# Performance work log

Hardware: AMD Instinct MI355X
Metric: run time of the kernel (lower is better)

The kernel has to match this reference:

```python
import jax, jax.numpy as jnp
import numpy as np

R = 32
LORA_ALPHA = 64
SCALING = LORA_ALPHA / R  # 2.0
TOPK = 2
NOISE_EPS = 0.01


def setup_inputs() -> dict:
    key = jax.random.key(0)
    ks = jax.random.split(key, 7)
    B, S, D, OUT, E = 4, 2048, 4096, 4096, 8
    x = jax.random.normal(ks[0], (B, S, D), dtype=jnp.float32)
    eof_index = jax.random.randint(ks[1], (B,), 0, S)
    noise = jax.random.normal(ks[2], (B, E), dtype=jnp.float32)
    # learned params (random instead of the zero-init in reset_parameters so the
    # output is non-trivial); Linear weight layout is [out_features, in_features]
    A_w = jax.random.normal(ks[3], (R, D), dtype=jnp.float32) * (1.0 / np.sqrt(D))
    B_w = jax.random.normal(ks[4], (E, OUT, R), dtype=jnp.float32) * (1.0 / np.sqrt(R))
    route_w = jax.random.normal(ks[5], (E, D), dtype=jnp.float32) * (1.0 / np.sqrt(D))
    noise_w = jax.random.normal(ks[6], (E, D), dtype=jnp.float32) * (1.0 / np.sqrt(D))
    return {"x": x, "eof_index": eof_index, "noise": noise,
            "A_w": A_w, "B_w": B_w, "route_w": route_w, "noise_w": noise_w}


def reference(x, eof_index, noise, A_w, B_w, route_w, noise_w):
    B = x.shape[0]
    rows = jnp.arange(B)
    # routing input: token at eof_index for each batch row -> [B, D]
    routing_input = x[rows, eof_index]
    # noisy top-k gating (training path: noisy_gating and is_train are True)
    clean_logits = routing_input @ route_w.T                       # [B, E]
    noise_stddev = jax.nn.softplus(routing_input @ noise_w.T) + NOISE_EPS
    logits = clean_logits + noise * noise_stddev                   # [B, E]
    # torch code takes topk+1 then slices to topk; equivalent to top_k(topk)
    top_vals, top_idx = jax.lax.top_k(logits, TOPK)                # [B, K]
    top_gates = jax.nn.softmax(top_vals.astype(jnp.float32), axis=-1).astype(x.dtype)
    gates = jnp.zeros_like(logits).at[rows[:, None], top_idx].set(top_gates)  # [B, E]
    # shared low-rank projection
    shared = jnp.einsum('bsd,rd->bsr', x, A_w)                     # [B, S, r]
    # sum_i gate_i * (shared @ B_i^T), fused as one contraction
    lora_output = jnp.einsum('bsr,eor,be->bso', shared, B_w, gates)  # [B, S, out]
    return lora_output * SCALING
```

## Files before the change

### kernel.cpp

```cpp
#include <hip/hip_runtime.h>
#include <stdint.h>
#include <math.h>

#define B_ 4
#define S_ 2048
#define D_ 4096
#define O_ 4096
#define E_ 8
#define R_ 32
#define SCALING 2.0f
#define NOISE_EPS 0.01f

typedef unsigned short u16;
typedef short s16x8 __attribute__((ext_vector_type(8)));
typedef float f32x4 __attribute__((ext_vector_type(4)));

__device__ __forceinline__ float b2f(u16 u) {
  union { unsigned int i; float f; } v; v.i = ((unsigned int)u) << 16; return v.f;
}
__device__ __forceinline__ u16 f2b(float f) {
  union { unsigned int i; float f; } v; v.f = f;
  unsigned int i = v.i;
  return (u16)((i + 0x7FFFu + ((i >> 16) & 1u)) >> 16);
}
__device__ __forceinline__ void split2(float f, u16* h, u16* l) {
  u16 hi = f2b(f);
  *h = hi;
  *l = f2b(f - b2f(hi));
}

__device__ __forceinline__ float ld(const void* p, size_t i, int bf) {
  return bf ? b2f(((const u16*)p)[i]) : ((const float*)p)[i];
}

__global__ void k_detect(const unsigned int* __restrict__ xw, int* __restrict__ flag) {
  __shared__ int cnt;
  if (threadIdx.x == 0) cnt = 0;
  __syncthreads();
  unsigned int w = xw[threadIdx.x];
  unsigned int e = (w >> 7) & 0xFFu;
  if (e >= 90u && e <= 140u) atomicAdd(&cnt, 1);
  __syncthreads();
  if (threadIdx.x == 0) *flag = (cnt > 48) ? 1 : 0;
}

__global__ __launch_bounds__(256) void k_logits(
    const void* __restrict__ x, const int* __restrict__ eof,
    const void* __restrict__ route_w, const void* __restrict__ noise_w,
    const int* __restrict__ flag, float* __restrict__ wsf) {
  int bf = *flag;
  int be = blockIdx.x;
  int b = be >> 3, e = be & 7;
  size_t xoff = ((size_t)b * S_ + (size_t)eof[b]) * D_;
  size_t woff = (size_t)e * D_;
  float ac = 0.f, an = 0.f;
  for (int d = threadIdx.x; d < D_; d += 256) {
    float xv = ld(x, xoff + d, bf);
    ac += xv * ld(route_w, woff + d, bf);
    an += xv * ld(noise_w, woff + d, bf);
  }
  __shared__ float rc[256], rn[256];
  rc[threadIdx.x] = ac; rn[threadIdx.x] = an;
  __syncthreads();
  for (int s = 128; s > 0; s >>= 1) {
    if (threadIdx.x < (unsigned)s) {
      rc[threadIdx.x] += rc[threadIdx.x + s];
      rn[threadIdx.x] += rn[threadIdx.x + s];
    }
    __syncthreads();
  }
  if (threadIdx.x == 0) { wsf[16 + be] = rc[0]; wsf[48 + be] = rn[0]; }
}

__global__ void k_gates(const void* __restrict__ noise, const int* __restrict__ flag,
                        float* __restrict__ wsf) {
  int bf = *flag;
  int b = threadIdx.x;
  if (b >= B_) return;
  float lg[E_];
  for (int e = 0; e < E_; e++) {
    float c = wsf[16 + b * 8 + e];
    float n = wsf[48 + b * 8 + e];
    float sp = (n > 20.f) ? n : log1pf(expf(n));
    lg[e] = c + ld(noise, b * 8 + e, bf) * (sp + NOISE_EPS);
  }
  int i1 = 0; float v1 = lg[0];
  for (int e = 1; e < E_; e++) if (lg[e] > v1) { v1 = lg[e]; i1 = e; }
  int i2 = -1; float v2 = -3.0e38f;
  for (int e = 0; e < E_; e++) if (e != i1 && lg[e] > v2) { v2 = lg[e]; i2 = e; }
  float t = expf(v2 - v1);
  float g1 = 1.f / (1.f + t);
  float g2 = t / (1.f + t);
  for (int e = 0; e < E_; e++) wsf[80 + b * 8 + e] = 0.f;
  wsf[80 + b * 8 + i1] = g1;
  wsf[80 + b * 8 + i2] = g2;
}

__global__ __launch_bounds__(256) void k_prepA(
    const float* __restrict__ Aw, const int* __restrict__ flag,
    u16* __restrict__ A2h, u16* __restrict__ A2l) {
  if (*flag) return;
  int idx = blockIdx.x * 256 + threadIdx.x;
  f32x4 v = ((const f32x4*)Aw)[idx];
  ushort4 h, l;
  split2(v[0], &h.x, &l.x); split2(v[1], &h.y, &l.y);
  split2(v[2], &h.z, &l.z); split2(v[3], &h.w, &l.w);
  ((ushort4*)A2h)[idx] = h;
  ((ushort4*)A2l)[idx] = l;
}

__global__ __launch_bounds__(256) void k_wc(
    const void* __restrict__ Bw, const int* __restrict__ flag,
    const float* __restrict__ gates, u16* __restrict__ Wc2h,
    u16* __restrict__ Wc2l) {
  int bf = *flag;
  int idx = blockIdx.x * 256 + threadIdx.x;
  int b = idx >> 15;
  int u = idx & 32767;
  float g[E_];
#pragma unroll
  for (int e = 0; e < E_; e++) g[e] = gates[b * 8 + e];
  f32x4 acc = {0.f, 0.f, 0.f, 0.f};
  if (bf) {
#pragma unroll
    for (int e = 0; e < E_; e++) {
      ushort4 v = ((const ushort4*)Bw)[(size_t)e * 32768 + u];
      acc[0] += g[e] * b2f(v.x);
      acc[1] += g[e] * b2f(v.y);
      acc[2] += g[e] * b2f(v.z);
      acc[3] += g[e] * b2f(v.w);
    }
  } else {
#pragma unroll
    for (int e = 0; e < E_; e++) {
      f32x4 v = ((const f32x4*)Bw)[(size_t)e * 32768 + u];
      acc += g[e] * v;
    }
  }
  acc *= SCALING;
  ushort4 h, l;
  split2(acc[0], &h.x, &l.x); split2(acc[1], &h.y, &l.y);
  split2(acc[2], &h.z, &l.z); split2(acc[3], &h.w, &l.w);
  ((ushort4*)Wc2h)[idx] = h;
  ((ushort4*)Wc2l)[idx] = l;
}

__global__ __launch_bounds__(256) void k_sharedM(
    const void* __restrict__ xv, const void* __restrict__ Awv,
    const u16* __restrict__ A2h, const u16* __restrict__ A2l,
    const int* __restrict__ flag, u16* __restrict__ sh2h,
    u16* __restrict__ sh2l) {
  __shared__ float red[4][512];
  int bf = *flag;
  int lane = threadIdx.x & 63;
  int wave = threadIdx.x >> 6;
  int m = lane & 15, kg = lane >> 4;
  int row0 = blockIdx.x * 16;
  int kbase = wave * 1024 + kg * 8;
  f32x4 acc0 = {0.f, 0.f, 0.f, 0.f};
  f32x4 acc1 = {0.f, 0.f, 0.f, 0.f};
  if (bf) {
    const u16* xp = (const u16*)xv + (size_t)(row0 + m) * D_ + kbase;
    const u16* a0 = (const u16*)Awv + (size_t)m * D_ + kbase;
    const u16* a1 = (const u16*)Awv + (size_t)(m + 16) * D_ + kbase;
#pragma unroll 4
    for (int k0 = 0; k0 < 1024; k0 += 32) {
      s16x8 a  = *(const s16x8*)(xp + k0);
      s16x8 b0 = *(const s16x8*)(a0 + k0);
      s16x8 b1 = *(const s16x8*)(a1 + k0);
      acc0 = __builtin_amdgcn_mfma_f32_16x16x32_bf16(a, b0, acc0, 0, 0, 0);
      acc1 = __builtin_amdgcn_mfma_f32_16x16x32_bf16(a, b1, acc1, 0, 0, 0);
    }
  } else {
    const float* xp = (const float*)xv + (size_t)(row0 + m) * D_ + kbase;
    const u16* h0 = A2h + (size_t)m * D_ + kbase;
    const u16* l0 = A2l + (size_t)m * D_ + kbase;
    const u16* h1 = A2h + (size_t)(m + 16) * D_ + kbase;
    const u16* l1 = A2l + (size_t)(m + 16) * D_ + kbase;
#pragma unroll 2
    for (int k0 = 0; k0 < 1024; k0 += 32) {
      f32x4 x0 = *(const f32x4*)(xp + k0);
      f32x4 x1 = *(const f32x4*)(xp + k0 + 4);
      s16x8 xh, xl;
      u16 hh, ll;
#pragma unroll
      for (int j = 0; j < 4; j++) {
        split2(x0[j], &hh, &ll); xh[j] = (short)hh; xl[j] = (short)ll;
        split2(x1[j], &hh, &ll); xh[j + 4] = (short)hh; xl[j + 4] = (short)ll;
      }
      s16x8 bh0 = *(const s16x8*)(h0 + k0);
      s16x8 bl0 = *(const s16x8*)(l0 + k0);
      s16x8 bh1 = *(const s16x8*)(h1 + k0);
      s16x8 bl1 = *(const s16x8*)(l1 + k0);
      acc0 = __builtin_amdgcn_mfma_f32_16x16x32_bf16(xh, bh0, acc0, 0, 0, 0);
      acc0 = __builtin_amdgcn_mfma_f32_16x16x32_bf16(xh, bl0, acc0, 0, 0, 0);
      acc0 = __builtin_amdgcn_mfma_f32_16x16x32_bf16(xl, bh0, acc0, 0, 0, 0);
      acc1 = __builtin_amdgcn_mfma_f32_16x16x32_bf16(xh, bh1, acc1, 0, 0, 0);
      acc1 = __builtin_amdgcn_mfma_f32_16x16x32_bf16(xh, bl1, acc1, 0, 0, 0);
      acc1 = __builtin_amdgcn_mfma_f32_16x16x32_bf16(xl, bh1, acc1, 0, 0, 0);
    }
  }
  int crow = (lane >> 4) * 4, ccol = lane & 15;
#pragma unroll
  for (int j = 0; j < 4; j++) {
    red[wave][(crow + j) * 32 + ccol]      = acc0[j];
    red[wave][(crow + j) * 32 + ccol + 16] = acc1[j];
  }
  __syncthreads();
  int t = threadIdx.x;
#pragma unroll
  for (int q = 0; q < 2; q++) {
    int e = t + q * 256;
    float s = red[0][e] + red[1][e] + red[2][e] + red[3][e];
    u16 h, l;
    split2(s, &h, &l);
    sh2h[(size_t)row0 * R_ + e] = h;
    sh2l[(size_t)row0 * R_ + e] = l;
  }
}

__global__ __launch_bounds__(256) void k_outM(
    const u16* __restrict__ sh2h, const u16* __restrict__ sh2l,
    const u16* __restrict__ Wc2h, const u16* __restrict__ Wc2l,
    const int* __restrict__ flag, void* __restrict__ out) {
  int bf = *flag;
  int lane = threadIdx.x & 63;
  int wave = threadIdx.x >> 6;
  int rb = blockIdx.x >> 5;
  int ob = blockIdx.x & 31;
  int row0 = rb * 64 + wave * 16;
  int b = row0 >> 11;
  int m = lane & 15, kg = lane >> 4;
  s16x8 Ah = *(const s16x8*)(sh2h + (size_t)(row0 + m) * R_ + kg * 8);
  s16x8 Al = *(const s16x8*)(sh2l + (size_t)(row0 + m) * R_ + kg * 8);
  const u16* wh = Wc2h + (size_t)b * (O_ * R_) + (size_t)(ob * 128 + m) * R_ + kg * 8;
  const u16* wl = Wc2l + (size_t)b * (O_ * R_) + (size_t)(ob * 128 + m) * R_ + kg * 8;
  int crow = (lane >> 4) * 4;
#pragma unroll
  for (int ot = 0; ot < 8; ot++) {
    s16x8 Bh = *(const s16x8*)(wh + (size_t)ot * 16 * R_);
    s16x8 Bl = *(const s16x8*)(wl + (size_t)ot * 16 * R_);
    f32x4 acc = {0.f, 0.f, 0.f, 0.f};
    acc = __builtin_amdgcn_mfma_f32_16x16x32_bf16(Ah, Bh, acc, 0, 0, 0);
    acc = __builtin_amdgcn_mfma_f32_16x16x32_bf16(Ah, Bl, acc, 0, 0, 0);
    acc = __builtin_amdgcn_mfma_f32_16x16x32_bf16(Al, Bh, acc, 0, 0, 0);
    int o = ob * 128 + ot * 16 + m;
    if (bf) {
      u16* op = (u16*)out + (size_t)(row0 + crow) * O_ + o;
#pragma unroll
      for (int j = 0; j < 4; j++) op[(size_t)j * O_] = f2b(acc[j]);
    } else {
      float* op = (float*)out + (size_t)(row0 + crow) * O_ + o;
#pragma unroll
      for (int j = 0; j < 4; j++) op[(size_t)j * O_] = acc[j];
    }
  }
}

extern "C" void kernel_launch(void* const* d_in, const int* in_sizes, int n_in,
                              void* d_out, int out_size, void* d_ws, size_t ws_size,
                              hipStream_t stream) {
  const void* x       = d_in[0];
  const int*  eof     = (const int*)d_in[1];
  const void* noise   = d_in[2];
  const void* Aw      = d_in[3];
  const void* Bw      = d_in[4];
  const void* route_w = d_in[5];
  const void* noise_w = d_in[6];
  float* wsf = (float*)d_ws;
  int* flag = (int*)wsf;
  float* gates = wsf + 80;
  u16* Wc2h = (u16*)(wsf + 112);
  u16* Wc2l = Wc2h + (size_t)B_ * O_ * R_;
  u16* A2h  = Wc2l + (size_t)B_ * O_ * R_;
  u16* A2l  = A2h + (size_t)R_ * D_;
  u16* sh2h = A2l + (size_t)R_ * D_;
  u16* sh2l = sh2h + (size_t)B_ * S_ * R_;

  k_detect<<<1, 64, 0, stream>>>((const unsigned int*)x, flag);
  k_logits<<<B_ * E_, 256, 0, stream>>>(x, eof, route_w, noise_w, flag, wsf);
  k_gates<<<1, 64, 0, stream>>>(noise, flag, wsf);
  k_prepA<<<(R_ * D_ / 4) / 256, 256, 0, stream>>>((const float*)Aw, flag, A2h, A2l);
  k_wc<<<(B_ * O_ * R_ / 4) / 256, 256, 0, stream>>>(Bw, flag, gates, Wc2h, Wc2l);
  k_sharedM<<<(B_ * S_) / 16, 256, 0, stream>>>(x, Aw, A2h, A2l, flag, sh2h, sh2l);
  k_outM<<<((B_ * S_) / 64) * (O_ / 128), 256, 0, stream>>>(
      sh2h, sh2l, Wc2h, Wc2l, flag, d_out);
}
```

Measured before the change: 318.5 us.

## Prepack MFMA operand layouts, stage x through swizzled LDS, coalesce output stores

A and the gate-combined B weights are now written in MFMA fragment order, so each lane reads its 16-byte operand contiguously. k_sharedM stages fp32 x rows into swizzled LDS as bf16 hi/lo with coalesced global reads. It then runs the split-bf16 MFMA chain over k-chunks, and writes shared in fragment layout. k_outM now handles 16 rows per block across all output columns, staging results in LDS so stores are wide and coalesced. The cost is extra block barriers and LDS use, plus a different grid shape.

```diff
diff --git a/kernel.cpp b/kernel.cpp
--- a/kernel.cpp
+++ b/kernel.cpp
@@ -98,25 +98,38 @@
 
 __global__ __launch_bounds__(256) void k_prepA(
     const float* __restrict__ Aw, const int* __restrict__ flag,
-    u16* __restrict__ A2h, u16* __restrict__ A2l) {
+    u16* __restrict__ Aph, u16* __restrict__ Apl) {
   if (*flag) return;
-  int idx = blockIdx.x * 256 + threadIdx.x;
-  f32x4 v = ((const f32x4*)Aw)[idx];
-  ushort4 h, l;
-  split2(v[0], &h.x, &l.x); split2(v[1], &h.y, &l.y);
-  split2(v[2], &h.z, &l.z); split2(v[3], &h.w, &l.w);
-  ((ushort4*)A2h)[idx] = h;
-  ((ushort4*)A2l)[idx] = l;
+  int flat = blockIdx.x * 256 + threadIdx.x;
+  int k32idx = flat >> 7;
+  int rem = flat & 127;
+  int h = rem >> 6;
+  int lane = rem & 63;
+  int r = h * 16 + (lane & 15);
+  int d = k32idx * 32 + (lane >> 4) * 8;
+  const float* src = Aw + (size_t)r * D_ + d;
+  f32x4 v0 = *(const f32x4*)src;
+  f32x4 v1 = *(const f32x4*)(src + 4);
+  ushort4 h0, l0, h1, l1;
+  split2(v0[0], &h0.x, &l0.x); split2(v0[1], &h0.y, &l0.y);
+  split2(v0[2], &h0.z, &l0.z); split2(v0[3], &h0.w, &l0.w);
+  split2(v1[0], &h1.x, &l1.x); split2(v1[1], &h1.y, &l1.y);
+  split2(v1[2], &h1.z, &l1.z); split2(v1[3], &h1.w, &l1.w);
+  *(ushort4*)(Aph + (size_t)flat * 8)     = h0;
+  *(ushort4*)(Aph + (size_t)flat * 8 + 4) = h1;
+  *(ushort4*)(Apl + (size_t)flat * 8)     = l0;
+  *(ushort4*)(Apl + (size_t)flat * 8 + 4) = l1;
 }
 
 __global__ __launch_bounds__(256) void k_wc(
     const void* __restrict__ Bw, const int* __restrict__ flag,
-    const float* __restrict__ gates, u16* __restrict__ Wc2h,
-    u16* __restrict__ Wc2l) {
+    const float* __restrict__ gates, u16* __restrict__ Wph,
+    u16* __restrict__ Wpl) {
   int bf = *flag;
   int idx = blockIdx.x * 256 + threadIdx.x;
   int b = idx >> 15;
   int u = idx & 32767;
+  int o = u >> 3, rq = u & 7;
   float g[E_];
 #pragma unroll
   for (int e = 0; e < E_; e++) g[e] = gates[b * 8 + e];
@@ -141,25 +154,31 @@
   ushort4 h, l;
   split2(acc[0], &h.x, &l.x); split2(acc[1], &h.y, &l.y);
   split2(acc[2], &h.z, &l.z); split2(acc[3], &h.w, &l.w);
-  ((ushort4*)Wc2h)[idx] = h;
-  ((ushort4*)Wc2l)[idx] = l;
+  int ot = o >> 4;
+  int lane = ((rq >> 1) * 16) + (o & 15);
+  size_t base = (((size_t)b * 256 + ot) * 64 + lane) * 8 + (rq & 1) * 4;
+  *(ushort4*)(Wph + base) = h;
+  *(ushort4*)(Wpl + base) = l;
 }
 
 __global__ __launch_bounds__(256) void k_sharedM(
     const void* __restrict__ xv, const void* __restrict__ Awv,
-    const u16* __restrict__ A2h, const u16* __restrict__ A2l,
+    const u16* __restrict__ Aph, const u16* __restrict__ Apl,
     const int* __restrict__ flag, u16* __restrict__ sh2h,
     u16* __restrict__ sh2l) {
+  __shared__ u16 xh[4096];
+  __shared__ u16 xl[4096];
   __shared__ float red[4][512];
   int bf = *flag;
-  int lane = threadIdx.x & 63;
-  int wave = threadIdx.x >> 6;
+  int t = threadIdx.x;
+  int lane = t & 63;
+  int wave = t >> 6;
   int m = lane & 15, kg = lane >> 4;
   int row0 = blockIdx.x * 16;
-  int kbase = wave * 1024 + kg * 8;
   f32x4 acc0 = {0.f, 0.f, 0.f, 0.f};
   f32x4 acc1 = {0.f, 0.f, 0.f, 0.f};
   if (bf) {
+    int kbase = wave * 1024 + kg * 8;
     const u16* xp = (const u16*)xv + (size_t)(row0 + m) * D_ + kbase;
     const u16* a0 = (const u16*)Awv + (size_t)m * D_ + kbase;
     const u16* a1 = (const u16*)Awv + (size_t)(m + 16) * D_ + kbase;
@@ -172,33 +191,45 @@
       acc1 = __builtin_amdgcn_mfma_f32_16x16x32_bf16(a, b1, acc1, 0, 0, 0);
     }
   } else {
-    const float* xp = (const float*)xv + (size_t)(row0 + m) * D_ + kbase;
-    const u16* h0 = A2h + (size_t)m * D_ + kbase;
-    const u16* l0 = A2l + (size_t)m * D_ + kbase;
-    const u16* h1 = A2h + (size_t)(m + 16) * D_ + kbase;
-    const u16* l1 = A2l + (size_t)(m + 16) * D_ + kbase;
-#pragma unroll 2
-    for (int k0 = 0; k0 < 1024; k0 += 32) {
-      f32x4 x0 = *(const f32x4*)(xp + k0);
-      f32x4 x1 = *(const f32x4*)(xp + k0 + 4);
-      s16x8 xh, xl;
-      u16 hh, ll;
-#pragma unroll
-      for (int j = 0; j < 4; j++) {
-        split2(x0[j], &hh, &ll); xh[j] = (short)hh; xl[j] = (short)ll;
-        split2(x1[j], &hh, &ll); xh[j + 4] = (short)hh; xl[j + 4] = (short)ll;
+    int srow = t >> 4;
+    int sq = t & 15;
+    const float* xrow = (const float*)xv + (size_t)(row0 + srow) * D_;
+    for (int kc = 0; kc < D_; kc += 256) {
+      __syncthreads();
+#pragma unroll
+      for (int q = 0; q < 4; q++) {
+        int colf = (sq + q * 16) * 4;
+        f32x4 v = *(const f32x4*)(xrow + kc + colf);
+        ushort4 h, l;
+        split2(v[0], &h.x, &l.x); split2(v[1], &h.y, &l.y);
+        split2(v[2], &h.z, &l.z); split2(v[3], &h.w, &l.w);
+        int swz = (srow * 512 + colf * 2) ^ ((srow & 7) << 4);
+        *(ushort4*)((char*)xh + swz) = h;
+        *(ushort4*)((char*)xl + swz) = l;
       }
-      s16x8 bh0 = *(const s16x8*)(h0 + k0);
-      s16x8 bl0 = *(const s16x8*)(l0 + k0);
-      s16x8 bh1 = *(const s16x8*)(h1 + k0);
-      s16x8 bl1 = *(const s16x8*)(l1 + k0);
-      acc0 = __builtin_amdgcn_mfma_f32_16x16x32_bf16(xh, bh0, acc0, 0, 0, 0);
-      acc0 = __builtin_amdgcn_mfma_f32_16x16x32_bf16(xh, bl0, acc0, 0, 0, 0);
-      acc0 = __builtin_amdgcn_mfma_f32_16x16x32_bf16(xl, bh0, acc0, 0, 0, 0);
-      acc1 = __builtin_amdgcn_mfma_f32_16x16x32_bf16(xh, bh1, acc1, 0, 0, 0);
-      acc1 = __builtin_amdgcn_mfma_f32_16x16x32_bf16(xh, bl1, acc1, 0, 0, 0);
-      acc1 = __builtin_amdgcn_mfma_f32_16x16x32_bf16(xl, bh1, acc1, 0, 0, 0);
-    }
+      __syncthreads();
+#pragma unroll
+      for (int p = 0; p < 2; p++) {
+        int k32 = (wave * 2 + p) * 32;
+        int boff = (m * 512 + (k32 + kg * 8) * 2) ^ ((m & 7) << 4);
+        s16x8 ah = *(const s16x8*)((const char*)xh + boff);
+        s16x8 al = *(const s16x8*)((const char*)xl + boff);
+        size_t k32idx = (size_t)(kc >> 5) + wave * 2 + p;
+        const u16* ph = Aph + (k32idx * 2) * 512;
+        const u16* pl = Apl + (k32idx * 2) * 512;
+        s16x8 bh0 = *(const s16x8*)(ph + (size_t)lane * 8);
+        s16x8 bl0 = *(const s16x8*)(pl + (size_t)lane * 8);
+        s16x8 bh1 = *(const s16x8*)(ph + 512 + (size_t)lane * 8);
+        s16x8 bl1 = *(const s16x8*)(pl + 512 + (size_t)lane * 8);
+        acc0 = __builtin_amdgcn_mfma_f32_16x16x32_bf16(ah, bh0, acc0, 0, 0, 0);
+        acc0 = __builtin_amdgcn_mfma_f32_16x16x32_bf16(ah, bl0, acc0, 0, 0, 0);
+        acc0 = __builtin_amdgcn_mfma_f32_16x16x32_bf16(al, bh0, acc0, 0, 0, 0);
+        acc1 = __builtin_amdgcn_mfma_f32_16x16x32_bf16(ah, bh1, acc1, 0, 0, 0);
+        acc1 = __builtin_amdgcn_mfma_f32_16x16x32_bf16(ah, bl1, acc1, 0, 0, 0);
+        acc1 = __builtin_amdgcn_mfma_f32_16x16x32_bf16(al, bh1, acc1, 0, 0, 0);
+      }
+    }
+    __syncthreads();
   }
   int crow = (lane >> 4) * 4, ccol = lane & 15;
 #pragma unroll
@@ -207,53 +238,67 @@
     red[wave][(crow + j) * 32 + ccol + 16] = acc1[j];
   }
   __syncthreads();
-  int t = threadIdx.x;
 #pragma unroll
   for (int q = 0; q < 2; q++) {
     int e = t + q * 256;
     float s = red[0][e] + red[1][e] + red[2][e] + red[3][e];
     u16 h, l;
     split2(s, &h, &l);
-    sh2h[(size_t)row0 * R_ + e] = h;
-    sh2l[(size_t)row0 * R_ + e] = l;
-  }
-}
-
+    int row = e >> 5, r = e & 31;
+    size_t dst = (size_t)blockIdx.x * 512 + ((size_t)(r >> 3) * 16 + row) * 8 + (r & 7);
+    sh2h[dst] = h;
+    sh2l[dst] = l;
+  }
+}
+
+#define OCH 512
 __global__ __launch_bounds__(256) void k_outM(
     const u16* __restrict__ sh2h, const u16* __restrict__ sh2l,
-    const u16* __restrict__ Wc2h, const u16* __restrict__ Wc2l,
+    const u16* __restrict__ Wph, const u16* __restrict__ Wpl,
     const int* __restrict__ flag, void* __restrict__ out) {
-  int bf = *flag;
-  int lane = threadIdx.x & 63;
-  int wave = threadIdx.x >> 6;
-  int rb = blockIdx.x >> 5;
-  int ob = blockIdx.x & 31;
-  int row0 = rb * 64 + wave * 16;
+  __shared__ float C[16][516];
+  int bf = *flag;
+  int t = threadIdx.x;
+  int lane = t & 63, wave = t >> 6;
+  int row0 = blockIdx.x * 16;
   int b = row0 >> 11;
-  int m = lane & 15, kg = lane >> 4;
-  s16x8 Ah = *(const s16x8*)(sh2h + (size_t)(row0 + m) * R_ + kg * 8);
-  s16x8 Al = *(const s16x8*)(sh2l + (size_t)(row0 + m) * R_ + kg * 8);
-  const u16* wh = Wc2h + (size_t)b * (O_ * R_) + (size_t)(ob * 128 + m) * R_ + kg * 8;
-  const u16* wl = Wc2l + (size_t)b * (O_ * R_) + (size_t)(ob * 128 + m) * R_ + kg * 8;
+  int m = lane & 15;
+  s16x8 Ah = *(const s16x8*)(sh2h + (size_t)blockIdx.x * 512 + (size_t)lane * 8);
+  s16x8 Al = *(const s16x8*)(sh2l + (size_t)blockIdx.x * 512 + (size_t)lane * 8);
   int crow = (lane >> 4) * 4;
-#pragma unroll
-  for (int ot = 0; ot < 8; ot++) {
-    s16x8 Bh = *(const s16x8*)(wh + (size_t)ot * 16 * R_);
-    s16x8 Bl = *(const s16x8*)(wl + (size_t)ot * 16 * R_);
-    f32x4 acc = {0.f, 0.f, 0.f, 0.f};
-    acc = __builtin_amdgcn_mfma_f32_16x16x32_bf16(Ah, Bh, acc, 0, 0, 0);
-    acc = __builtin_amdgcn_mfma_f32_16x16x32_bf16(Ah, Bl, acc, 0, 0, 0);
-    acc = __builtin_amdgcn_mfma_f32_16x16x32_bf16(Al, Bh, acc, 0, 0, 0);
-    int o = ob * 128 + ot * 16 + m;
-    if (bf) {
-      u16* op = (u16*)out + (size_t)(row0 + crow) * O_ + o;
-#pragma unroll
-      for (int j = 0; j < 4; j++) op[(size_t)j * O_] = f2b(acc[j]);
-    } else {
-      float* op = (float*)out + (size_t)(row0 + crow) * O_ + o;
-#pragma unroll
-      for (int j = 0; j < 4; j++) op[(size_t)j * O_] = acc[j];
-    }
+  const u16* whB = Wph + (size_t)b * 131072;
+  const u16* wlB = Wpl + (size_t)b * 131072;
+  for (int oc = 0; oc < O_; oc += OCH) {
+#pragma unroll
+    for (int i = 0; i < 8; i++) {
+      int otc = wave * 8 + i;
+      size_t otg = (size_t)((oc >> 4) + otc);
+      s16x8 Bh = *(const s16x8*)(whB + otg * 512 + (size_t)lane * 8);
+      s16x8 Bl = *(const s16x8*)(wlB + otg * 512 + (size_t)lane * 8);
+      f32x4 acc = {0.f, 0.f, 0.f, 0.f};
+      acc = __builtin_amdgcn_mfma_f32_16x16x32_bf16(Ah, Bh, acc, 0, 0, 0);
+      acc = __builtin_amdgcn_mfma_f32_16x16x32_bf16(Ah, Bl, acc, 0, 0, 0);
+      acc = __builtin_amdgcn_mfma_f32_16x16x32_bf16(Al, Bh, acc, 0, 0, 0);
+      int ocol = otc * 16 + m;
+#pragma unroll
+      for (int j = 0; j < 4; j++) C[crow + j][ocol] = acc[j];
+    }
+    __syncthreads();
+#pragma unroll
+    for (int it = 0; it < 8; it++) {
+      int row = it * 2 + (t >> 7);
+      int col = (t & 127) * 4;
+      f32x4 v = *(const f32x4*)&C[row][col];
+      size_t off = (size_t)(row0 + row) * O_ + oc + col;
+      if (bf) {
+        ushort4 o4;
+        o4.x = f2b(v[0]); o4.y = f2b(v[1]); o4.z = f2b(v[2]); o4.w = f2b(v[3]);
+        *(ushort4*)((u16*)out + off) = o4;
+      } else {
+        *(f32x4*)((float*)out + off) = v;
+      }
+    }
+    __syncthreads();
   }
 }
 
@@ -270,19 +315,18 @@
   float* wsf = (float*)d_ws;
   int* flag = (int*)wsf;
   float* gates = wsf + 80;
-  u16* Wc2h = (u16*)(wsf + 112);
-  u16* Wc2l = Wc2h + (size_t)B_ * O_ * R_;
-  u16* A2h  = Wc2l + (size_t)B_ * O_ * R_;
-  u16* A2l  = A2h + (size_t)R_ * D_;
-  u16* sh2h = A2l + (size_t)R_ * D_;
+  u16* Wph  = (u16*)(wsf + 112);
+  u16* Wpl  = Wph + (size_t)B_ * O_ * R_;
+  u16* Aph  = Wpl + (size_t)B_ * O_ * R_;
+  u16* Apl  = Aph + (size_t)R_ * D_;
+  u16* sh2h = Apl + (size_t)R_ * D_;
   u16* sh2l = sh2h + (size_t)B_ * S_ * R_;
 
   k_detect<<<1, 64, 0, stream>>>((const unsigned int*)x, flag);
   k_logits<<<B_ * E_, 256, 0, stream>>>(x, eof, route_w, noise_w, flag, wsf);
   k_gates<<<1, 64, 0, stream>>>(noise, flag, wsf);
-  k_prepA<<<(R_ * D_ / 4) / 256, 256, 0, stream>>>((const float*)Aw, flag, A2h, A2l);
-  k_wc<<<(B_ * O_ * R_ / 4) / 256, 256, 0, stream>>>(Bw, flag, gates, Wc2h, Wc2l);
-  k_sharedM<<<(B_ * S_) / 16, 256, 0, stream>>>(x, Aw, A2h, A2l, flag, sh2h, sh2l);
-  k_outM<<<((B_ * S_) / 64) * (O_ / 128), 256, 0, stream>>>(
-      sh2h, sh2l, Wc2h, Wc2l, flag, d_out);
-}
+  k_prepA<<<64, 256, 0, stream>>>((const float*)Aw, flag, Aph, Apl);
+  k_wc<<<(B_ * O_ * R_ / 4) / 256, 256, 0, stream>>>(Bw, flag, gates, Wph, Wpl);
+  k_sharedM<<<(B_ * S_) / 16, 256, 0, stream>>>(x, Aw, Aph, Apl, flag, sh2h, sh2l);
+  k_outM<<<(B_ * S_) / 16, 256, 0, stream>>>(sh2h, sh2l, Wph, Wpl, flag, d_out);
+}
```

Result: no change. 315.1 us (-1.0%).
